# Kernel tuning notes

Measured on AMD Instinct MI355X. Metric: run time of the kernel, lower is better.

Reference implementation:

```python
import jax, jax.numpy as jnp
import numpy as np
import math

B, C, DH = 2048, 64, 512
CAP_VOCAB = 11  # max(core_capacities)+1
DIST_VOCAB = 3


def setup_inputs() -> dict:
    key = jax.random.key(0)
    ks = jax.random.split(key, 12)
    inp = {
        "Ht_C": jax.random.normal(ks[0], (B, C, DH), jnp.float32),
        "core_capacities": jax.random.randint(ks[1], (B, C), 0, CAP_VOCAB),
        "distances": jax.random.randint(ks[2], (B, C), 0, DIST_VOCAB),
        "H_X": jax.random.normal(ks[3], (B, DH), jnp.float32),
        "Ht_S": jax.random.normal(ks[4], (B, DH), jnp.float32),
        "Eq_Q": jax.random.normal(ks[5], (B, DH), jnp.float32),
        "double": jax.random.randint(ks[6], (B,), 0, 2).astype(bool),
        # learned parameters (nn.Embedding tables and bias-free Linear weights, [out,in])
        "cap_emb": jax.random.normal(ks[7], (CAP_VOCAB, DH), jnp.float32) * 0.02,
        "dist_emb": jax.random.normal(ks[8], (DIST_VOCAB, DH), jnp.float32) * 0.02,
        "W_q": jax.random.normal(ks[9], (DH, 3 * DH), jnp.float32) * (1.0 / math.sqrt(3 * DH)),
        "W_k": jax.random.normal(ks[10], (DH, DH), jnp.float32) * (1.0 / math.sqrt(DH)),
        "W_v": jax.random.normal(ks[11], (DH, DH), jnp.float32) * (1.0 / math.sqrt(DH)),
    }
    return inp


def reference(Ht_C, core_capacities, distances, H_X, Ht_S, Eq_Q, double,
              cap_emb, dist_emb, W_q, W_k, W_v):
    scale = 1.0 / math.sqrt(Ht_C.shape[-1])  # 1/sqrt(d_H), slice_emb_size == d_H
    # dynamic core embeddings G_{t,q}^{(C)}: [B,C,dH]
    G = Ht_C + cap_emb[core_capacities] + dist_emb[distances]
    # context and projections
    context = jnp.concatenate([H_X, Ht_S, Eq_Q], axis=-1)          # [B,3dH]
    Q = context @ W_q.T                                            # [B,dH]
    K = jnp.einsum('bcd,ed->bce', G, W_k)                          # [B,C,dH]
    V = jnp.einsum('bcd,ed->bce', G, W_v)                          # [B,C,dH]
    # glimpse attention over cores
    attn_logits = jnp.einsum('bcd,bd->bc', K, Q) * scale           # [B,C]
    attn_weights = jax.nn.softmax(attn_logits, axis=-1)            # softmax over cores
    glimpse = jnp.einsum('bc,bcd->bd', attn_weights, V)            # [B,dH]
    # pointer logits + capacity mask
    u = jnp.einsum('bcd,bd->bc', K, glimpse) * scale               # [B,C]
    need = jnp.where(double[:, None], 2, 1)                        # [B,1]
    invalid = core_capacities < need                               # [B,C]
    u = jnp.where(invalid, -jnp.inf, u)
    return jax.nn.softmax(u, axis=-1)                              # [B,C]
```

## Files before the change

kernel.cpp:

```cpp
#include <hip/hip_runtime.h>
#include <math.h>

#define DH 512
#define CC 64
#define NB 2048
#define SCALE 0.044194173824159216f

__device__ __forceinline__ float wsum(float v) {
#pragma unroll
  for (int off = 32; off; off >>= 1) v += __shfl_xor(v, off, 64);
  return v;
}

__global__ __launch_bounds__(128) void pre_kernel(const float* __restrict__ Wq,
                                                  const float* __restrict__ Wv,
                                                  const float* __restrict__ Wk,
                                                  float* __restrict__ Aout,
                                                  float* __restrict__ Mout,
                                                  const unsigned char* __restrict__ dbl,
                                                  int* __restrict__ need) {
  const int bx = blockIdx.x;
  const int t = threadIdx.x;
  if (bx == 256) {
    __shared__ int flagNZ, flagFP;
    if (t == 0) { flagNZ = 0; flagFP = 0; }
    __syncthreads();
    int nz = 0, fp = 0;
    for (int i = t; i < NB; i += 128) {
      if (i & 3) {
        unsigned char v = dbl[i];
        nz |= (v != 0);
        fp |= (v == 0x3f) | (v == 0x80);
      }
    }
    if (nz) atomicOr(&flagNZ, 1);
    if (fp) atomicOr(&flagFP, 1);
    __syncthreads();
    const int isFP = flagFP, isByte = flagNZ && !flagFP;
    for (int i = t; i < NB; i += 128) {
      int v;
      if (isFP)        v = (((const float*)dbl)[i] != 0.0f);
      else if (isByte) v = (dbl[i] != 0);
      else             v = (((const int*)dbl)[i] != 0);
      need[i] = v ? 2 : 1;
    }
    return;
  }
  __shared__ float As[16][64];
  __shared__ float Bs[16][64];
  const int mt = bx >> 3, nt = bx & 7;
  const int m0 = mt * 64, n0 = nt * 64;
  const bool isQ = (m0 < 1536);
  const float* Acol = isQ ? (Wq + m0) : (Wv + (m0 - 1536));
  const int lda = isQ ? 1536 : 512;
  float* Cout = isQ ? (Aout + (size_t)m0 * 512) : (Mout + (size_t)(m0 - 1536) * 512);
  const int lr = t >> 3;
  const int lc = (t & 7) << 3;
  const int tx = t & 15, ty = t >> 4;

  float4 ra0, ra1, rb0, rb1;
  ra0 = *(const float4*)&Acol[(size_t)lr * lda + lc];
  ra1 = *(const float4*)&Acol[(size_t)lr * lda + lc + 4];
  rb0 = *(const float4*)&Wk[(size_t)lr * 512 + n0 + lc];
  rb1 = *(const float4*)&Wk[(size_t)lr * 512 + n0 + lc + 4];
  float acc[8][4] = {};
  for (int k0 = 0; k0 < 512; k0 += 16) {
    __syncthreads();
    *(float4*)&As[lr][lc] = ra0;
    *(float4*)&As[lr][lc + 4] = ra1;
    *(float4*)&Bs[lr][lc] = rb0;
    *(float4*)&Bs[lr][lc + 4] = rb1;
    __syncthreads();
    if (k0 + 16 < 512) {
      const int kn = k0 + 16 + lr;
      ra0 = *(const float4*)&Acol[(size_t)kn * lda + lc];
      ra1 = *(const float4*)&Acol[(size_t)kn * lda + lc + 4];
      rb0 = *(const float4*)&Wk[(size_t)kn * 512 + n0 + lc];
      rb1 = *(const float4*)&Wk[(size_t)kn * 512 + n0 + lc + 4];
    }
#pragma unroll
    for (int k = 0; k < 16; ++k) {
      float4 a0 = *(float4*)&As[k][ty << 3];
      float4 a1 = *(float4*)&As[k][(ty << 3) + 4];
      float4 b  = *(float4*)&Bs[k][tx << 2];
      float av[8] = {a0.x, a0.y, a0.z, a0.w, a1.x, a1.y, a1.z, a1.w};
      float bv[4] = {b.x, b.y, b.z, b.w};
#pragma unroll
      for (int i = 0; i < 8; ++i)
#pragma unroll
        for (int j = 0; j < 4; ++j) acc[i][j] = fmaf(av[i], bv[j], acc[i][j]);
    }
  }
#pragma unroll
  for (int i = 0; i < 8; ++i) {
    float4 o = {acc[i][0], acc[i][1], acc[i][2], acc[i][3]};
    *(float4*)&Cout[(size_t)((ty << 3) + i) * 512 + n0 + (tx << 2)] = o;
  }
}

#define AS_STR 132

__global__ __launch_bounds__(256) void gemm_nn2p(const float* __restrict__ A0,
                                                 const float* __restrict__ A1,
                                                 const float* __restrict__ A2,
                                                 const float* __restrict__ B,
                                                 float* __restrict__ Cp,
                                                 int kchunk) {
  __shared__ float As[16 * AS_STR];
  __shared__ float Bs[16 * 64];
  const int t = threadIdx.x;
  const int m0 = blockIdx.x * 128, n0 = blockIdx.y * 64;
  const int kbeg = blockIdx.z * kchunk, kend = kbeg + kchunk;
  float* C = Cp + (size_t)blockIdx.z * (NB * DH);
  const int tx = t & 15, ty = t >> 4;
  const int ar0 = t >> 2;
  const int ak4 = (t & 3) << 2;
  const int bk = t >> 4, bn4 = (t & 15) << 2;

  float4 ra0, ra1, rb;
  {
    const float* base = (kbeg < 512) ? A0 : ((kbeg < 1024) ? A1 : A2);
    const int kk = kbeg & 511;
    ra0 = *(const float4*)&base[(size_t)(m0 + ar0) * 512 + kk + ak4];
    ra1 = *(const float4*)&base[(size_t)(m0 + ar0 + 64) * 512 + kk + ak4];
    rb  = *(const float4*)&B[(size_t)(kbeg + bk) * 512 + n0 + bn4];
  }
  float acc[8][4] = {};
  for (int k0 = kbeg; k0 < kend; k0 += 16) {
    __syncthreads();
    As[(ak4 + 0) * AS_STR + ar0] = ra0.x;
    As[(ak4 + 1) * AS_STR + ar0] = ra0.y;
    As[(ak4 + 2) * AS_STR + ar0] = ra0.z;
    As[(ak4 + 3) * AS_STR + ar0] = ra0.w;
    As[(ak4 + 0) * AS_STR + ar0 + 64] = ra1.x;
    As[(ak4 + 1) * AS_STR + ar0 + 64] = ra1.y;
    As[(ak4 + 2) * AS_STR + ar0 + 64] = ra1.z;
    As[(ak4 + 3) * AS_STR + ar0 + 64] = ra1.w;
    *(float4*)&Bs[bk * 64 + bn4] = rb;
    __syncthreads();
    if (k0 + 16 < kend) {
      const int kn = k0 + 16;
      const float* base = (kn < 512) ? A0 : ((kn < 1024) ? A1 : A2);
      const int kk = kn & 511;
      ra0 = *(const float4*)&base[(size_t)(m0 + ar0) * 512 + kk + ak4];
      ra1 = *(const float4*)&base[(size_t)(m0 + ar0 + 64) * 512 + kk + ak4];
      rb  = *(const float4*)&B[(size_t)(kn + bk) * 512 + n0 + bn4];
    }
#pragma unroll
    for (int k = 0; k < 16; ++k) {
      float4 a0 = *(float4*)&As[k * AS_STR + (ty << 3)];
      float4 a1 = *(float4*)&As[k * AS_STR + (ty << 3) + 4];
      float4 b  = *(float4*)&Bs[k * 64 + (tx << 2)];
      float av[8] = {a0.x, a0.y, a0.z, a0.w, a1.x, a1.y, a1.z, a1.w};
      float bv[4] = {b.x, b.y, b.z, b.w};
#pragma unroll
      for (int i = 0; i < 8; ++i)
#pragma unroll
        for (int j = 0; j < 4; ++j) acc[i][j] = fmaf(av[i], bv[j], acc[i][j]);
    }
  }
#pragma unroll
  for (int i = 0; i < 8; ++i) {
    float4 o = {acc[i][0], acc[i][1], acc[i][2], acc[i][3]};
    *(float4*)&C[(size_t)(m0 + (ty << 3) + i) * 512 + n0 + (tx << 2)] = o;
  }
}

__global__ __launch_bounds__(256, 4) void fused_kernel(const float* __restrict__ HtC,
                                                       const int* __restrict__ caps,
                                                       const int* __restrict__ dists,
                                                       const float* __restrict__ Qkp,
                                                       const float* __restrict__ Mm,
                                                       const float* __restrict__ cap_emb,
                                                       const float* __restrict__ dist_emb,
                                                       const int* __restrict__ need,
                                                       float* __restrict__ out) {
  const int t = threadIdx.x;
  const int wv = t >> 6, ln = t & 63;
  const int b0 = blockIdx.x << 1;

  __shared__ float qk[2][DH];
  __shared__ float Gws[2][DH];
  __shared__ float gks[2][DH];
  __shared__ float gkp[2][2][DH];
  __shared__ float accs[4][DH];
  __shared__ float ec[CC];
  __shared__ float capQ[2][11], distQ[2][3];
  __shared__ float capE[11], distE[3];
  __shared__ float capG[2][11], distG[2][3];
  __shared__ float lsum_s;

#pragma unroll
  for (int h = 0; h < 2; ++h) {
    const size_t bo = (size_t)(b0 + h) * DH;
    float q0 = 0.f, q1 = 0.f;
#pragma unroll
    for (int z = 0; z < 4; ++z) {
      q0 += Qkp[(size_t)z * NB * DH + bo + t];
      q1 += Qkp[(size_t)z * NB * DH + bo + 256 + t];
    }
    qk[h][t] = q0;
    qk[h][t + 256] = q1;
  }
  __syncthreads();

#pragma unroll
  for (int h = 0; h < 2; ++h) {
#pragma unroll
    for (int r = 0; r < 3; ++r) {
      int v = wv + (r << 2);
      if (v < 11) {
        float s = 0.f;
#pragma unroll
        for (int j = 0; j < 8; ++j) s = fmaf(cap_emb[v * DH + ln + (j << 6)], qk[h][ln + (j << 6)], s);
        s = wsum(s);
        if (ln == 0) capQ[h][v] = s;
      }
    }
    if (wv < 3) {
      float s = 0.f;
#pragma unroll
      for (int j = 0; j < 8; ++j) s = fmaf(dist_emb[wv * DH + ln + (j << 6)], qk[h][ln + (j << 6)], s);
      s = wsum(s);
      if (ln == 0) distQ[h][wv] = s;
    }
  }

  for (int h = 0; h < 2; ++h) {
    const int b = b0 + h;
    if (t < 11) capE[t] = 0.f;
    if (t < 3) distE[t] = 0.f;
    __syncthreads();
    const float4* qk4 = (const float4*)qk[h];
    float4 q1 = qk4[ln];
    float4 q2 = qk4[64 + ln];
    const float* hb = HtC + (size_t)b * CC * DH;
    float a0 = 0.f, a1 = 0.f, a2 = 0.f, a3 = 0.f, a4 = 0.f, a5 = 0.f, a6 = 0.f, a7 = 0.f;
#pragma unroll 4
    for (int i = 0; i < 16; ++i) {
      int c = (wv << 4) + i;
      const float4* h4 = (const float4*)(hb + (size_t)c * DH);
      float4 h1 = h4[ln];
      float4 h2 = h4[64 + ln];
      float s = h1.x * q1.x + h1.y * q1.y + h1.z * q1.z + h1.w * q1.w +
                h2.x * q2.x + h2.y * q2.y + h2.z * q2.z + h2.w * q2.w;
      s = wsum(s);
      float logit = SCALE * (s + capQ[h][caps[b * CC + c]] + distQ[h][dists[b * CC + c]]);
      float e = __expf(logit);
      if (ln == 0) ec[c] = e;
      a0 = fmaf(e, h1.x, a0); a1 = fmaf(e, h1.y, a1);
      a2 = fmaf(e, h1.z, a2); a3 = fmaf(e, h1.w, a3);
      a4 = fmaf(e, h2.x, a4); a5 = fmaf(e, h2.y, a5);
      a6 = fmaf(e, h2.z, a6); a7 = fmaf(e, h2.w, a7);
    }
    {
      int d0 = ln << 2;
      accs[wv][d0 + 0] = a0; accs[wv][d0 + 1] = a1;
      accs[wv][d0 + 2] = a2; accs[wv][d0 + 3] = a3;
      accs[wv][256 + d0 + 0] = a4; accs[wv][256 + d0 + 1] = a5;
      accs[wv][256 + d0 + 2] = a6; accs[wv][256 + d0 + 3] = a7;
    }
    __syncthreads();
    if (t < CC) {
      float e = ec[t];
      float l = wsum(e);
      if (t == 0) lsum_s = l;
      atomicAdd(&capE[caps[b * CC + t]], e);
      atomicAdd(&distE[dists[b * CC + t]], e);
    }
    __syncthreads();
    const float rinv = 1.0f / lsum_s;
#pragma unroll
    for (int dd = 0; dd < 2; ++dd) {
      int d = t + (dd << 8);
      float g = accs[0][d] + accs[1][d] + accs[2][d] + accs[3][d];
#pragma unroll
      for (int v = 0; v < 11; ++v) g = fmaf(capE[v], cap_emb[v * DH + d], g);
#pragma unroll
      for (int v = 0; v < 3; ++v) g = fmaf(distE[v], dist_emb[v * DH + d], g);
      Gws[h][d] = g * rinv;
    }
    __syncthreads();
  }

  {
    const int e4 = (t & 127) << 2;
    const int half = t >> 7;
    const float* Mp = Mm + (size_t)(half << 8) * DH + e4;
    const float* g0p = &Gws[0][half << 8];
    const float* g1p = &Gws[1][half << 8];
    float s00 = 0.f, s01 = 0.f, s02 = 0.f, s03 = 0.f;
    float s10 = 0.f, s11 = 0.f, s12 = 0.f, s13 = 0.f;
#pragma unroll 8
    for (int d = 0; d < 256; ++d) {
      float4 m4 = *(const float4*)&Mp[(size_t)d * DH];
      float g0 = g0p[d];
      float g1 = g1p[d];
      s00 = fmaf(g0, m4.x, s00); s01 = fmaf(g0, m4.y, s01);
      s02 = fmaf(g0, m4.z, s02); s03 = fmaf(g0, m4.w, s03);
      s10 = fmaf(g1, m4.x, s10); s11 = fmaf(g1, m4.y, s11);
      s12 = fmaf(g1, m4.z, s12); s13 = fmaf(g1, m4.w, s13);
    }
    gkp[half][0][e4 + 0] = s00; gkp[half][0][e4 + 1] = s01;
    gkp[half][0][e4 + 2] = s02; gkp[half][0][e4 + 3] = s03;
    gkp[half][1][e4 + 0] = s10; gkp[half][1][e4 + 1] = s11;
    gkp[half][1][e4 + 2] = s12; gkp[half][1][e4 + 3] = s13;
  }
  __syncthreads();
#pragma unroll
  for (int h = 0; h < 2; ++h) {
    gks[h][t] = gkp[0][h][t] + gkp[1][h][t];
    gks[h][t + 256] = gkp[0][h][t + 256] + gkp[1][h][t + 256];
  }
  __syncthreads();

#pragma unroll
  for (int h = 0; h < 2; ++h) {
#pragma unroll
    for (int r = 0; r < 3; ++r) {
      int v = wv + (r << 2);
      if (v < 11) {
        float s = 0.f;
#pragma unroll
        for (int j = 0; j < 8; ++j) s = fmaf(cap_emb[v * DH + ln + (j << 6)], gks[h][ln + (j << 6)], s);
        s = wsum(s);
        if (ln == 0) capG[h][v] = s;
      }
    }
    if (wv < 3) {
      float s = 0.f;
#pragma unroll
      for (int j = 0; j < 8; ++j) s = fmaf(dist_emb[wv * DH + ln + (j << 6)], gks[h][ln + (j << 6)], s);
      s = wsum(s);
      if (ln == 0) distG[h][wv] = s;
    }
  }
  __syncthreads();

  for (int h = 1; h >= 0; --h) {
    const int b = b0 + h;
    const float4* gk4 = (const float4*)gks[h];
    float4 q1 = gk4[ln];
    float4 q2 = gk4[64 + ln];
    const float* hb = HtC + (size_t)b * CC * DH;
#pragma unroll 4
    for (int i = 0; i < 16; ++i) {
      int c = (wv << 4) + i;
      const float4* h4 = (const float4*)(hb + (size_t)c * DH);
      float4 h1 = h4[ln];
      float4 h2 = h4[64 + ln];
      float s = h1.x * q1.x + h1.y * q1.y + h1.z * q1.z + h1.w * q1.w +
                h2.x * q2.x + h2.y * q2.y + h2.z * q2.z + h2.w * q2.w;
      s = wsum(s);
      if (ln == 0)
        ec[c] = SCALE * (s + capG[h][caps[b * CC + c]] + distG[h][dists[b * CC + c]]);
    }
    __syncthreads();
    if (t < CC) {
      int nb = need[b];
      float x = ec[t];
      if (caps[b * CC + t] < nb) x = -INFINITY;
      float m = x;
#pragma unroll
      for (int off = 32; off; off >>= 1) m = fmaxf(m, __shfl_xor(m, off, 64));
      float e = __expf(x - m);
      float ssum = wsum(e);
      out[(size_t)b * CC + t] = e / ssum;
    }
    __syncthreads();
  }
}

extern "C" void kernel_launch(void* const* d_in, const int* in_sizes, int n_in,
                              void* d_out, int out_size, void* d_ws, size_t ws_size,
                              hipStream_t stream) {
  const float* HtC      = (const float*)d_in[0];
  const int* caps       = (const int*)d_in[1];
  const int* dists      = (const int*)d_in[2];
  const float* H_X      = (const float*)d_in[3];
  const float* Ht_S     = (const float*)d_in[4];
  const float* Eq_Q     = (const float*)d_in[5];
  const unsigned char* dbl = (const unsigned char*)d_in[6];
  const float* cap_emb  = (const float*)d_in[7];
  const float* dist_emb = (const float*)d_in[8];
  const float* W_q      = (const float*)d_in[9];
  const float* W_k      = (const float*)d_in[10];
  const float* W_v      = (const float*)d_in[11];
  float* out = (float*)d_out;

  float* ws     = (float*)d_ws;
  float* wsA    = ws;
  float* wsM    = wsA + 1536 * 512;
  float* wsQkp  = wsM + 512 * 512;
  int* wsNeed   = (int*)(wsQkp + 4 * 2048 * 512);

  pre_kernel<<<257, 128, 0, stream>>>(W_q, W_v, W_k, wsA, wsM, dbl, wsNeed);
  gemm_nn2p<<<dim3(16, 8, 4), 256, 0, stream>>>(H_X, Ht_S, Eq_Q, wsA, wsQkp, 384);
  fused_kernel<<<NB / 2, 256, 0, stream>>>(HtC, caps, dists, wsQkp, wsM,
                                           cap_emb, dist_emb, wsNeed, out);
}
```

Before: 536.3 us.

## Batch HtC loads and shuffle reductions across cores; stage caps/dists in LDS

Restructures the per-core loops so all 16 row dot products are loaded and computed before their wave reductions run together. This exposes more independent memory loads and shuffle chains in flight at once, where before each iteration serialized load, reduce and exp. The glimpse accumulation now re-reads the HtC rows in a second pass, which adds global or cache traffic and register pressure from the 16-entry arrays. Core capacity and distance indices are also staged once into shared memory instead of being read repeatedly from global memory.

```diff
diff --git a/kernel.cpp b/kernel.cpp
--- a/kernel.cpp
+++ b/kernel.cpp
@@ -189,6 +189,13 @@
   __shared__ float capE[11], distE[3];
   __shared__ float capG[2][11], distG[2][3];
   __shared__ float lsum_s;
+  __shared__ int capsS[2][CC], distsS[2][CC];
+
+  if (t < 128) {
+    int hh = t >> 6, c = t & 63;
+    capsS[hh][c] = caps[(size_t)(b0 + hh) * CC + c];
+    distsS[hh][c] = dists[(size_t)(b0 + hh) * CC + c];
+  }
 
 #pragma unroll
   for (int h = 0; h < 2; ++h) {
@@ -235,23 +242,43 @@
     float4 q1 = qk4[ln];
     float4 q2 = qk4[64 + ln];
     const float* hb = HtC + (size_t)b * CC * DH;
-    float a0 = 0.f, a1 = 0.f, a2 = 0.f, a3 = 0.f, a4 = 0.f, a5 = 0.f, a6 = 0.f, a7 = 0.f;
-#pragma unroll 4
+
+    float sp[16];
+#pragma unroll
+    for (int g = 0; g < 2; ++g) {
+#pragma unroll
+      for (int i = 0; i < 8; ++i) {
+        const int c = (wv << 4) + (g << 3) + i;
+        const float4* h4 = (const float4*)(hb + (size_t)c * DH);
+        float4 h1 = h4[ln];
+        float4 h2 = h4[64 + ln];
+        sp[(g << 3) + i] = h1.x * q1.x + h1.y * q1.y + h1.z * q1.z + h1.w * q1.w +
+                           h2.x * q2.x + h2.y * q2.y + h2.z * q2.z + h2.w * q2.w;
+      }
+    }
+#pragma unroll
+    for (int i = 0; i < 16; ++i) sp[i] = wsum(sp[i]);
+    float ei[16];
+#pragma unroll
     for (int i = 0; i < 16; ++i) {
       int c = (wv << 4) + i;
-      const float4* h4 = (const float4*)(hb + (size_t)c * DH);
+      float logit = SCALE * (sp[i] + capQ[h][capsS[h][c]] + distQ[h][distsS[h][c]]);
+      ei[i] = __expf(logit);
+    }
+    if (ln == 0) {
+#pragma unroll
+      for (int i = 0; i < 16; ++i) ec[(wv << 4) + i] = ei[i];
+    }
+    float a0 = 0.f, a1 = 0.f, a2 = 0.f, a3 = 0.f, a4 = 0.f, a5 = 0.f, a6 = 0.f, a7 = 0.f;
+#pragma unroll
+    for (int i = 0; i < 16; ++i) {
+      const float4* h4 = (const float4*)(hb + (size_t)((wv << 4) + i) * DH);
       float4 h1 = h4[ln];
       float4 h2 = h4[64 + ln];
-      float s = h1.x * q1.x + h1.y * q1.y + h1.z * q1.z + h1.w * q1.w +
-                h2.x * q2.x + h2.y * q2.y + h2.z * q2.z + h2.w * q2.w;
-      s = wsum(s);
-      float logit = SCALE * (s + capQ[h][caps[b * CC + c]] + distQ[h][dists[b * CC + c]]);
-      float e = __expf(logit);
-      if (ln == 0) ec[c] = e;
-      a0 = fmaf(e, h1.x, a0); a1 = fmaf(e, h1.y, a1);
-      a2 = fmaf(e, h1.z, a2); a3 = fmaf(e, h1.w, a3);
-      a4 = fmaf(e, h2.x, a4); a5 = fmaf(e, h2.y, a5);
-      a6 = fmaf(e, h2.z, a6); a7 = fmaf(e, h2.w, a7);
+      a0 = fmaf(ei[i], h1.x, a0); a1 = fmaf(ei[i], h1.y, a1);
+      a2 = fmaf(ei[i], h1.z, a2); a3 = fmaf(ei[i], h1.w, a3);
+      a4 = fmaf(ei[i], h2.x, a4); a5 = fmaf(ei[i], h2.y, a5);
+      a6 = fmaf(ei[i], h2.z, a6); a7 = fmaf(ei[i], h2.w, a7);
     }
     {
       int d0 = ln << 2;
@@ -265,8 +292,8 @@
       float e = ec[t];
       float l = wsum(e);
       if (t == 0) lsum_s = l;
-      atomicAdd(&capE[caps[b * CC + t]], e);
-      atomicAdd(&distE[dists[b * CC + t]], e);
+      atomicAdd(&capE[capsS[h][t]], e);
+      atomicAdd(&distE[distsS[h][t]], e);
     }
     __syncthreads();
     const float rinv = 1.0f / lsum_s;
@@ -343,23 +370,33 @@
     float4 q1 = gk4[ln];
     float4 q2 = gk4[64 + ln];
     const float* hb = HtC + (size_t)b * CC * DH;
-#pragma unroll 4
-    for (int i = 0; i < 16; ++i) {
-      int c = (wv << 4) + i;
-      const float4* h4 = (const float4*)(hb + (size_t)c * DH);
-      float4 h1 = h4[ln];
-      float4 h2 = h4[64 + ln];
-      float s = h1.x * q1.x + h1.y * q1.y + h1.z * q1.z + h1.w * q1.w +
-                h2.x * q2.x + h2.y * q2.y + h2.z * q2.z + h2.w * q2.w;
-      s = wsum(s);
-      if (ln == 0)
-        ec[c] = SCALE * (s + capG[h][caps[b * CC + c]] + distG[h][dists[b * CC + c]]);
+    float sp[16];
+#pragma unroll
+    for (int g = 0; g < 2; ++g) {
+#pragma unroll
+      for (int i = 0; i < 8; ++i) {
+        const int c = (wv << 4) + (g << 3) + i;
+        const float4* h4 = (const float4*)(hb + (size_t)c * DH);
+        float4 h1 = h4[ln];
+        float4 h2 = h4[64 + ln];
+        sp[(g << 3) + i] = h1.x * q1.x + h1.y * q1.y + h1.z * q1.z + h1.w * q1.w +
+                           h2.x * q2.x + h2.y * q2.y + h2.z * q2.z + h2.w * q2.w;
+      }
+    }
+#pragma unroll
+    for (int i = 0; i < 16; ++i) sp[i] = wsum(sp[i]);
+    if (ln == 0) {
+#pragma unroll
+      for (int i = 0; i < 16; ++i) {
+        int c = (wv << 4) + i;
+        ec[c] = SCALE * (sp[i] + capG[h][capsS[h][c]] + distG[h][distsS[h][c]]);
+      }
     }
     __syncthreads();
     if (t < CC) {
       int nb = need[b];
       float x = ec[t];
-      if (caps[b * CC + t] < nb) x = -INFINITY;
+      if (capsS[h][t] < nb) x = -INFINITY;
       float m = x;
 #pragma unroll
       for (int off = 32; off; off >>= 1) m = fmaxf(m, __shfl_xor(m, off, 64));
```

Measured after the change: 578.7 us. +7.9%, slower.
